# Performance work log

Measured on AMD Instinct MI355X. Metric: run time of the kernel, lower is better.

Reference implementation:

```python
import jax, jax.numpy as jnp
import numpy as np

B, C, RC, H, W = 4, 256, 128, 64, 64

def setup_inputs() -> dict:
    key = jax.random.key(0)
    ks = jax.random.split(key, 9)
    s = 0.05
    return {
        "x": jax.random.normal(ks[0], (B, C, H, W), jnp.float32),
        "wq": jax.random.normal(ks[1], (RC, C), jnp.float32) * s,
        "bq": jax.random.normal(ks[2], (RC,), jnp.float32) * s,
        "wk": jax.random.normal(ks[3], (RC, C), jnp.float32) * s,
        "bk": jax.random.normal(ks[4], (RC,), jnp.float32) * s,
        "wv": jax.random.normal(ks[5], (RC, C), jnp.float32) * s,
        "bv": jax.random.normal(ks[6], (RC,), jnp.float32) * s,
        "wo": jax.random.normal(ks[7], (C, RC), jnp.float32) * s,
        "bo": jax.random.normal(ks[8], (C,), jnp.float32) * s,
        "gamma": jnp.zeros((1,), jnp.float32) + 0.1,  # nonzero so output depends on attention
    }

def reference(x, wq, bq, wk, bk, wv, bv, wo, bo, gamma):
    b, c, h, w = x.shape
    n = h * w
    rc = wq.shape[0]
    xf = x.reshape(b, c, n)  # [B,C,N]
    # 1x1 convs == channel matmuls
    q = jnp.einsum('rc,bcn->bnr', wq, xf) + bq            # [B,N,RC]
    k = jnp.einsum('rc,bcn->brn', wk, xf) + bk[:, None]   # [B,RC,N]
    v = jnp.einsum('rc,bcn->bnr', wv, xf) + bv            # [B,N,RC]
    scale = rc ** -0.5
    attn = jax.nn.softmax(jnp.einsum('bnr,brm->bnm', q, k) * scale, axis=-1)  # [B,N,N]
    out = jnp.einsum('bnm,bmr->bnr', attn, v)             # [B,N,RC]
    out = jnp.einsum('cr,bnr->bcn', wo, out) + bo[None, :, None]  # [B,C,N]
    out = out.reshape(b, c, h, w)
    return gamma * out + x
```

## Files before the change

### kernel.cpp

```cpp
#include <hip/hip_runtime.h>
#include <hip/hip_bf16.h>


#define B_   4
#define C_   256
#define RC_  128
#define N_   4096
#define SCALEL 0.12750880597462906f

typedef __bf16 bf16x8 __attribute__((ext_vector_type(8)));
typedef unsigned short u16x8 __attribute__((ext_vector_type(8)));
typedef float f32x4 __attribute__((ext_vector_type(4)));

static __device__ __forceinline__ unsigned short f2bf(float f) {
    unsigned int u = __builtin_bit_cast(unsigned int, f);
    u += 0x7fffu + ((u >> 16) & 1u);
    return (unsigned short)(u >> 16);
}

static __device__ __forceinline__ f32x4 mfma16(u16x8 a, u16x8 b, f32x4 c) {
    return __builtin_amdgcn_mfma_f32_16x16x32_bf16(
        __builtin_bit_cast(bf16x8, a), __builtin_bit_cast(bf16x8, b), c, 0, 0, 0);
}

static __device__ __forceinline__ unsigned int cvtpk(float lo, float hi) {
    unsigned int r;
    asm("v_cvt_pk_bf16_f32 %0, %1, %2" : "=v"(r) : "v"(lo), "v"(hi));
    return r;
}

static __device__ __forceinline__ u16x8 ldw8(const float* p) {
    float4 f0 = *(const float4*)p;
    float4 f1 = *(const float4*)(p + 4);
    int4 pk;
    pk.x = (int)cvtpk(f0.x, f0.y);
    pk.y = (int)cvtpk(f0.z, f0.w);
    pk.z = (int)cvtpk(f1.x, f1.y);
    pk.w = (int)cvtpk(f1.z, f1.w);
    return __builtin_bit_cast(u16x8, pk);
}

static __device__ __forceinline__ int pk4fp8(float a, float b, float c, float d) {
    int w = __builtin_amdgcn_cvt_pk_fp8_f32(a, b, 0, false);
    w = __builtin_amdgcn_cvt_pk_fp8_f32(c, d, w, true);
    return w;
}

static __device__ __forceinline__ void gl_lds16(const void* g, void* l) {
    __builtin_amdgcn_global_load_lds(
        (const __attribute__((address_space(1))) void*)g,
        (__attribute__((address_space(3))) void*)l, 16, 0, 0);
}

#define K1_LDA 264

__global__ __launch_bounds__(256) void k_qkv(
    const float* __restrict__ x,
    const float* __restrict__ wq, const float* __restrict__ wk, const float* __restrict__ wv,
    const float* __restrict__ bq, const float* __restrict__ bk, const float* __restrict__ bv,
    unsigned char* __restrict__ Qf, unsigned char* __restrict__ Kf,
    unsigned char* __restrict__ Vt8)
{
    __shared__ unsigned short lds[32 * K1_LDA];
    const int b  = blockIdx.y;
    const int n0 = blockIdx.x * 32;
    const int t  = threadIdx.x;
    const int lane = t & 63, wv_ = t >> 6;
    const int g = lane >> 4, q16 = lane & 15;

    {
        int tk0 = (t & 7) * 4;
        int cb  = (t >> 3) * 8;
        const float* xb = x + ((size_t)b * C_ * N_) + n0 + tk0;
        float4 col[8];
        #pragma unroll
        for (int e = 0; e < 8; ++e)
            col[e] = *(const float4*)&xb[(size_t)(cb + e) * N_];
        #pragma unroll
        for (int tk = 0; tk < 4; ++tk) {
            u16x8 v;
            #pragma unroll
            for (int e = 0; e < 8; ++e) {
                float f = (tk == 0) ? col[e].x : (tk == 1) ? col[e].y
                        : (tk == 2) ? col[e].z : col[e].w;
                v[e] = f2bf(f);
            }
            *(u16x8*)&lds[(tk0 + tk) * K1_LDA + cb] = v;
        }
    }
    __syncthreads();

    f32x4 acc[3][2][2];
    #pragma unroll
    for (int tq = 0; tq < 3; ++tq)
        #pragma unroll
        for (int r2 = 0; r2 < 2; ++r2)
            #pragma unroll
            for (int nf = 0; nf < 2; ++nf)
                acc[tq][r2][nf] = (f32x4){0.f, 0.f, 0.f, 0.f};

    const float* wsrc[3] = {wq, wk, wv};
    const int rbase = wv_ * 32;
    #pragma unroll
    for (int ks = 0; ks < 8; ++ks) {
        u16x8 a[2];
        #pragma unroll
        for (int nf = 0; nf < 2; ++nf)
            a[nf] = *(const u16x8*)&lds[(nf * 16 + q16) * K1_LDA + ks * 32 + g * 8];
        #pragma unroll
        for (int tq = 0; tq < 3; ++tq) {
            const float* w = wsrc[tq];
            #pragma unroll
            for (int r2 = 0; r2 < 2; ++r2) {
                u16x8 bf = ldw8(&w[(size_t)(rbase + r2 * 16 + q16) * 256 + ks * 32 + g * 8]);
                #pragma unroll
                for (int nf = 0; nf < 2; ++nf) {
                    if (tq < 2)
                        acc[tq][r2][nf] = mfma16(bf, a[nf], acc[tq][r2][nf]);
                    else
                        acc[tq][r2][nf] = mfma16(a[nf], bf, acc[tq][r2][nf]);
                }
            }
        }
    }

    #pragma unroll
    for (int r2 = 0; r2 < 2; ++r2) {
        int rb = rbase + r2 * 16 + g * 4;
        float4 bq4 = *(const float4*)&bq[rb];
        float4 bk4 = *(const float4*)&bk[rb];
        #pragma unroll
        for (int nf = 0; nf < 2; ++nf) {
            int n = n0 + nf * 16 + q16;
            int qw32 = pk4fp8((acc[0][r2][nf][0] + bq4.x) * SCALEL,
                              (acc[0][r2][nf][1] + bq4.y) * SCALEL,
                              (acc[0][r2][nf][2] + bq4.z) * SCALEL,
                              (acc[0][r2][nf][3] + bq4.w) * SCALEL);
            int kw32 = pk4fp8(acc[1][r2][nf][0] + bk4.x, acc[1][r2][nf][1] + bk4.y,
                              acc[1][r2][nf][2] + bk4.z, acc[1][r2][nf][3] + bk4.w);
            size_t base = ((size_t)b * N_ + n) * RC_ + rb;
            *(unsigned int*)(Qf + base) = (unsigned int)qw32;
            *(unsigned int*)(Kf + base) = (unsigned int)kw32;
        }
    }

    const size_t tile = (size_t)b * 128 + blockIdx.x;
    #pragma unroll
    for (int r2 = 0; r2 < 2; ++r2) {
        int r = rbase + r2 * 16 + q16;
        float biasv = bv[r];
        #pragma unroll
        for (int nf = 0; nf < 2; ++nf) {
            int w = pk4fp8(acc[2][r2][nf][0] + biasv, acc[2][r2][nf][1] + biasv,
                           acc[2][r2][nf][2] + biasv, acc[2][r2][nf][3] + biasv);
            *(unsigned int*)(Vt8 + (tile * 128 + r) * 40 + g * 8 + nf * 4) = (unsigned int)w;
        }
    }
}

__global__ __launch_bounds__(1024, 4) void k_attn(
    const unsigned char* __restrict__ Qf, const unsigned char* __restrict__ Kf,
    const unsigned char* __restrict__ Vt8, unsigned short* __restrict__ Ob)
{
    __shared__ __align__(16) unsigned short smem[77824];
    const int b  = blockIdx.y;
    const int n0 = blockIdx.x * 64;
    const int t  = threadIdx.x;
    const int lane = t & 63, wv_ = t >> 6;
    const int qw = wv_ & 1, grp = wv_ >> 1;
    const int g = lane >> 4, q16 = lane & 15;

    unsigned char* Ql8 = (unsigned char*)smem;
    unsigned char* Klb = (unsigned char*)smem + 16384 + grp * 8192;
    unsigned char* Vl8 = (unsigned char*)smem + 81920 + grp * 5120;

    const unsigned char* Qg = Qf + ((size_t)b * N_ + n0) * RC_;
    const unsigned char* Kg = Kf + ((size_t)b * N_ + grp * 512) * RC_;
    const unsigned char* Vg = Vt8 + ((size_t)b * 128 + grp * 16) * 5120;

    if (t < 512) {
        int row = t >> 3, ch = t & 7;
        uint4 v = *(const uint4*)&Qg[row * 128 + ch * 16];
        *(uint4*)&Ql8[row * 128 + ((ch ^ (row & 7)) * 16)] = v;
    }

    #define STAGEK(kt_) do { int ktc = (kt_);                                    \
        _Pragma("unroll")                                                        \
        for (int r = 0; r < 2; ++r) {                                            \
            int id = (qw * 2 + r) * 64 + lane;         \
            int row = id >> 3, ch = id & 7;                                      \
            gl_lds16(Kg + (size_t)(ktc * 32 + row) * RC_ + ((ch ^ (row & 7)) * 16), \
                     Klb + (qw * 2 + r) * 1024);                                 \
        }                                                                        \
    } while (0)
    #define STAGEV(kt_) do { int ktc = (kt_);                                    \
        const char* vsrc = (const char*)(Vg + (size_t)ktc * 5120);               \
        char* vdst = (char*)Vl8;                                                 \
        _Pragma("unroll")                                                        \
        for (int j = 0; j < 2; ++j) {                                            \
            int off = j * 2048 + qw * 1024;                                      \
            gl_lds16(vsrc + off + lane * 16, vdst + off);                        \
        }                                                                        \
        if (qw == 0)                                                             \
            gl_lds16(vsrc + 4096 + lane * 16, vdst + 4096);                      \
    } while (0)

    STAGEK(0);
    STAGEV(0);

    f32x4 acc_o[2][8];
    #pragma unroll
    for (int rf = 0; rf < 2; ++rf)
        #pragma unroll
        for (int df = 0; df < 8; ++df)
            acc_o[rf][df] = (f32x4){0.f, 0.f, 0.f, 0.f};
    float l_loc[2] = {0.f, 0.f};

    __syncthreads();

    for (int kt = 0; kt < 16; ++kt) {
        f32x4 s[2][2];
        #pragma unroll
        for (int rf = 0; rf < 2; ++rf)
            #pragma unroll
            for (int kf = 0; kf < 2; ++kf)
                s[rf][kf] = (f32x4){0.f, 0.f, 0.f, 0.f};
        __builtin_amdgcn_s_setprio(1);
        #pragma unroll
        for (int ks = 0; ks < 4; ++ks) {
            int sw = (((2 * ks + (g >> 1)) ^ (q16 & 7)) * 16) + ((g & 1) * 8);
            long qv0 = *(const long*)&Ql8[(qw * 32 + q16) * 128 + sw];
            long qv1 = *(const long*)&Ql8[(qw * 32 + 16 + q16) * 128 + sw];
            #pragma unroll
            for (int kf = 0; kf < 2; ++kf) {
                long kv = *(const long*)&Klb[(kf * 16 + q16) * 128 + sw];
                s[0][kf] = __builtin_amdgcn_mfma_f32_16x16x32_fp8_fp8(kv, qv0, s[0][kf], 0, 0, 0);
                s[1][kf] = __builtin_amdgcn_mfma_f32_16x16x32_fp8_fp8(kv, qv1, s[1][kf], 0, 0, 0);
            }
        }
        __builtin_amdgcn_s_setprio(0);

        __syncthreads();
        if (kt < 15) STAGEK(kt + 1);

        long pa8[2];
        #pragma unroll
        for (int rf = 0; rf < 2; ++rf) {
            #pragma unroll
            for (int kf = 0; kf < 2; ++kf)
                #pragma unroll
                for (int i = 0; i < 4; ++i)
                    s[rf][kf][i] = exp2f(s[rf][kf][i]);
            l_loc[rf] += (s[rf][0][0] + s[rf][0][1]) + (s[rf][0][2] + s[rf][0][3])
                       + (s[rf][1][0] + s[rf][1][1]) + (s[rf][1][2] + s[rf][1][3]);
            int2 pk2;
            pk2.x = pk4fp8(s[rf][0][0], s[rf][0][1], s[rf][0][2], s[rf][0][3]);
            pk2.y = pk4fp8(s[rf][1][0], s[rf][1][1], s[rf][1][2], s[rf][1][3]);
            pa8[rf] = __builtin_bit_cast(long, pk2);
        }

        __builtin_amdgcn_s_setprio(1);
        #pragma unroll
        for (int df = 0; df < 8; ++df) {
            int d = df * 16 + q16;
            long vv = *(const long*)&Vl8[d * 40 + g * 8];
            acc_o[0][df] = __builtin_amdgcn_mfma_f32_16x16x32_fp8_fp8(pa8[0], vv, acc_o[0][df], 0, 0, 0);
            acc_o[1][df] = __builtin_amdgcn_mfma_f32_16x16x32_fp8_fp8(pa8[1], vv, acc_o[1][df], 0, 0, 0);
        }
        __builtin_amdgcn_s_setprio(0);

        __syncthreads();
        if (kt < 15) STAGEV(kt + 1);
    }

    float l0 = l_loc[0], l1 = l_loc[1];
    l0 += __shfl_xor(l0, 16); l0 += __shfl_xor(l0, 32);
    l1 += __shfl_xor(l1, 16); l1 += __shfl_xor(l1, 32);

    float* lf = (float*)smem;
    unsigned short* Ub = smem + 8192;
    if (g == 0) {
        lf[grp * 64 + qw * 32 + q16]      = l0;
        lf[grp * 64 + qw * 32 + 16 + q16] = l1;
    }
    {
        unsigned short* Ug = Ub + grp * 8448;
        #pragma unroll
        for (int rf = 0; rf < 2; ++rf)
            #pragma unroll
            for (int df = 0; df < 8; ++df)
                #pragma unroll
                for (int i = 0; i < 4; ++i)
                    Ug[(qw * 32 + rf * 16 + g * 4 + i) * 132 + df * 16 + q16] =
                        f2bf(acc_o[rf][df][i]);
    }
    __syncthreads();

    #pragma unroll
    for (int r = 0; r < 4; ++r) {
        int row = wv_ * 4 + r;
        float lt = 0.f;
        #pragma unroll
        for (int gg = 0; gg < 8; ++gg) lt += lf[gg * 64 + row];
        float inv = 1.f / lt;
        float o0 = 0.f, o1 = 0.f;
        #pragma unroll
        for (int gg = 0; gg < 8; ++gg) {
            unsigned int u = *(const unsigned int*)&Ub[gg * 8448 + row * 132 + lane * 2];
            o0 += __builtin_bit_cast(float, u << 16);
            o1 += __builtin_bit_cast(float, u & 0xffff0000u);
        }
        unsigned int packed = ((unsigned int)f2bf(o1 * inv) << 16) | f2bf(o0 * inv);
        *(unsigned int*)&Ob[((size_t)b * N_ + n0 + row) * RC_ + lane * 2] = packed;
    }
    #undef STAGEK
    #undef STAGEV
}

#define QS 136

__global__ __launch_bounds__(256) void k_out(
    const unsigned short* __restrict__ Ob, const float* __restrict__ wo,
    const float* __restrict__ bo, const float* __restrict__ x,
    const float* __restrict__ gamma, float* __restrict__ out)
{
    __shared__ unsigned short Ol[64 * QS];
    const int b  = blockIdx.z;
    const int c0 = blockIdx.y * 64;
    const int n0 = blockIdx.x * 64;
    const int t  = threadIdx.x;
    const int lane = t & 63, wv_ = t >> 6;
    const int g = lane >> 4, q16 = lane & 15;

    {
        const unsigned short* src = Ob + ((size_t)b * N_ + n0) * RC_;
        #pragma unroll
        for (int p = 0; p < 4; ++p) {
            int row = p * 16 + (t >> 4);
            int s = (t & 15) * 8;
            *(u16x8*)&Ol[row * QS + s] = *(const u16x8*)&src[row * RC_ + s];
        }
    }
    __syncthreads();

    f32x4 acc[4];
    #pragma unroll
    for (int nf = 0; nf < 4; ++nf)
        acc[nf] = (f32x4){0.f, 0.f, 0.f, 0.f};

    const int cw = c0 + wv_ * 16;
    #pragma unroll
    for (int ks = 0; ks < 4; ++ks) {
        u16x8 b8[4];
        #pragma unroll
        for (int nf = 0; nf < 4; ++nf)
            b8[nf] = *(const u16x8*)&Ol[(nf * 16 + q16) * QS + ks * 32 + g * 8];
        u16x8 a8 = ldw8(&wo[(size_t)(cw + q16) * 128 + ks * 32 + g * 8]);
        #pragma unroll
        for (int nf = 0; nf < 4; ++nf)
            acc[nf] = mfma16(a8, b8[nf], acc[nf]);
    }

    float gm = gamma[0];
    #pragma unroll
    for (int i = 0; i < 4; ++i) {
        int c = cw + g * 4 + i;
        float bias = bo[c];
        #pragma unroll
        for (int nf = 0; nf < 4; ++nf) {
            int n = n0 + nf * 16 + q16;
            size_t idx = ((size_t)b * C_ + c) * N_ + n;
            out[idx] = gm * (acc[nf][i] + bias) + x[idx];
        }
    }
}

extern "C" void kernel_launch(void* const* d_in, const int* in_sizes, int n_in,
                              void* d_out, int out_size, void* d_ws, size_t ws_size,
                              hipStream_t stream) {
    const float* x     = (const float*)d_in[0];
    const float* wq    = (const float*)d_in[1];
    const float* bq    = (const float*)d_in[2];
    const float* wk    = (const float*)d_in[3];
    const float* bk    = (const float*)d_in[4];
    const float* wv    = (const float*)d_in[5];
    const float* bv    = (const float*)d_in[6];
    const float* wo    = (const float*)d_in[7];
    const float* bo    = (const float*)d_in[8];
    const float* gamma = (const float*)d_in[9];
    float* out = (float*)d_out;

    unsigned char* wsb = (unsigned char*)d_ws;
    unsigned char* Qf  = wsb;
    unsigned char* Kf  = wsb + 2097152;
    unsigned char* Vt8 = wsb + 4194304;
    unsigned short* Ob = (unsigned short*)(wsb + 6815744);

    dim3 g1(128, 4);
    k_qkv<<<g1, 256, 0, stream>>>(x, wq, wk, wv, bq, bk, bv, Qf, Kf, Vt8);
    dim3 g2(64, 4);
    k_attn<<<g2, 1024, 0, stream>>>(Qf, Kf, Vt8, Ob);
    dim3 g3(64, 4, 4);
    k_out<<<g3, 256, 0, stream>>>(Ob, wo, bo, x, gamma, out);
}
```

Measured before the change: 84.18 us.

## Double-buffer K and V tiles in LDS to overlap loads with compute

Splits the K and V shared-memory staging areas into two ping-pong buffers. The next tile's K and V are issued at the top of each iteration, so the loads overlap the current QK and PV MFMAs. This drops one of the two block barriers per iteration. Q moves to a smaller region and the LDS layout is repacked to make room. The loop is unrolled by two so the buffer parity can be resolved at compile time.

```diff
diff --git a/kernel.cpp b/kernel.cpp
--- a/kernel.cpp
+++ b/kernel.cpp
@@ -171,8 +171,8 @@
     const int g = lane >> 4, q16 = lane & 15;
 
     unsigned char* Ql8 = (unsigned char*)smem;
-    unsigned char* Klb = (unsigned char*)smem + 16384 + grp * 8192;
-    unsigned char* Vl8 = (unsigned char*)smem + 81920 + grp * 5120;
+    unsigned char* Klb = (unsigned char*)smem + 8192 + grp * 8192;
+    unsigned char* Vlb = (unsigned char*)smem + 73728 + grp * 10240;
 
     const unsigned char* Qg = Qf + ((size_t)b * N_ + n0) * RC_;
     const unsigned char* Kg = Kf + ((size_t)b * N_ + grp * 512) * RC_;
@@ -184,18 +184,19 @@
         *(uint4*)&Ql8[row * 128 + ((ch ^ (row & 7)) * 16)] = v;
     }
 
-    #define STAGEK(kt_) do { int ktc = (kt_);                                    \
+    #define STAGEK(kt_, pb_) do { int ktc = (kt_);                               \
+        unsigned char* kdst = Klb + (pb_) * 4096;                                \
         _Pragma("unroll")                                                        \
         for (int r = 0; r < 2; ++r) {                                            \
             int id = (qw * 2 + r) * 64 + lane;         \
             int row = id >> 3, ch = id & 7;                                      \
             gl_lds16(Kg + (size_t)(ktc * 32 + row) * RC_ + ((ch ^ (row & 7)) * 16), \
-                     Klb + (qw * 2 + r) * 1024);                                 \
+                     kdst + (qw * 2 + r) * 1024);                                \
         }                                                                        \
     } while (0)
-    #define STAGEV(kt_) do { int ktc = (kt_);                                    \
+    #define STAGEV(kt_, pb_) do { int ktc = (kt_);                               \
         const char* vsrc = (const char*)(Vg + (size_t)ktc * 5120);               \
-        char* vdst = (char*)Vl8;                                                 \
+        char* vdst = (char*)(Vlb + (pb_) * 5120);                                \
         _Pragma("unroll")                                                        \
         for (int j = 0; j < 2; ++j) {                                            \
             int off = j * 2048 + qw * 1024;                                      \
@@ -205,8 +206,8 @@
             gl_lds16(vsrc + 4096 + lane * 16, vdst + 4096);                      \
     } while (0)
 
-    STAGEK(0);
-    STAGEV(0);
+    STAGEK(0, 0);
+    STAGEV(0, 0);
 
     f32x4 acc_o[2][8];
     #pragma unroll
@@ -218,7 +219,16 @@
 
     __syncthreads();
 
+    #pragma unroll 2
     for (int kt = 0; kt < 16; ++kt) {
+        const int p = kt & 1;
+        if (kt < 15) {
+            STAGEK(kt + 1, p ^ 1);
+            STAGEV(kt + 1, p ^ 1);
+        }
+        const unsigned char* Klp = Klb + p * 4096;
+        const unsigned char* Vlp = Vlb + p * 5120;
+
         f32x4 s[2][2];
         #pragma unroll
         for (int rf = 0; rf < 2; ++rf)
@@ -233,15 +243,12 @@
             long qv1 = *(const long*)&Ql8[(qw * 32 + 16 + q16) * 128 + sw];
             #pragma unroll
             for (int kf = 0; kf < 2; ++kf) {
-                long kv = *(const long*)&Klb[(kf * 16 + q16) * 128 + sw];
+                long kv = *(const long*)&Klp[(kf * 16 + q16) * 128 + sw];
                 s[0][kf] = __builtin_amdgcn_mfma_f32_16x16x32_fp8_fp8(kv, qv0, s[0][kf], 0, 0, 0);
                 s[1][kf] = __builtin_amdgcn_mfma_f32_16x16x32_fp8_fp8(kv, qv1, s[1][kf], 0, 0, 0);
             }
         }
         __builtin_amdgcn_s_setprio(0);
-
-        __syncthreads();
-        if (kt < 15) STAGEK(kt + 1);
 
         long pa8[2];
         #pragma unroll
@@ -263,14 +270,13 @@
         #pragma unroll
         for (int df = 0; df < 8; ++df) {
             int d = df * 16 + q16;
-            long vv = *(const long*)&Vl8[d * 40 + g * 8];
+            long vv = *(const long*)&Vlp[d * 40 + g * 8];
             acc_o[0][df] = __builtin_amdgcn_mfma_f32_16x16x32_fp8_fp8(pa8[0], vv, acc_o[0][df], 0, 0, 0);
             acc_o[1][df] = __builtin_amdgcn_mfma_f32_16x16x32_fp8_fp8(pa8[1], vv, acc_o[1][df], 0, 0, 0);
         }
         __builtin_amdgcn_s_setprio(0);
 
         __syncthreads();
-        if (kt < 15) STAGEV(kt + 1);
     }
 
     float l0 = l_loc[0], l1 = l_loc[1];
```

Result: faster. 81.43 us (-3.3%).
